# Performance work log

Measured on AMD Instinct MI355X. Metric: run time of the kernel, lower is better.

Reference implementation:

```python
import jax, jax.numpy as jnp
import numpy as np

B, L, D, N = 2, 2048, 1024, 16
HD = D // N  # head_dim = 64
EPS = 1e-5


def layer_norm(x, gamma, beta):
    mu = jnp.mean(x, axis=-1, keepdims=True)
    var = jnp.mean(jnp.square(x - mu), axis=-1, keepdims=True)
    return (x - mu) * jax.lax.rsqrt(var + EPS) * gamma + beta


def setup_inputs() -> dict:
    key = jax.random.key(0)
    ks = jax.random.split(key, 10)
    s = lambda fan_in: 1.0 / np.sqrt(fan_in)
    return {
        "x": jax.random.normal(ks[0], (B, L, D), dtype=jnp.float32),
        "wq": jax.random.uniform(ks[1], (D, D), jnp.float32, -s(D), s(D)),
        "wk": jax.random.uniform(ks[2], (D, D), jnp.float32, -s(D), s(D)),  # shared w_proj (k and v)
        "wo": jax.random.uniform(ks[3], (D, D), jnp.float32, -s(D), s(D)),
        "g1": jnp.ones((D,), jnp.float32),
        "b1": jnp.zeros((D,), jnp.float32),
        "w1": jax.random.uniform(ks[4], (D, 4 * D), jnp.float32, -s(D), s(D)),
        "bb1": jax.random.uniform(ks[5], (4 * D,), jnp.float32, -s(D), s(D)),
        "w2": jax.random.uniform(ks[6], (4 * D, D), jnp.float32, -s(4 * D), s(4 * D)),
        "bb2": jax.random.uniform(ks[7], (D,), jnp.float32, -s(4 * D), s(4 * D)),
        "g2": jnp.ones((D,), jnp.float32),
        "b2": jnp.zeros((D,), jnp.float32),
    }


def reference(x, wq, wk, wo, g1, b1, w1, bb1, w2, bb2, g2, b2):
    b, l, d = x.shape
    # projections (w_proj is shared for k and v in the source; v output is unused)
    q = (x @ wq).reshape(b, l, HD, N)
    k = (x @ wk).reshape(b, l, HD, N)
    # attention scores [b, l, m, n]; softmax over m (dim=2 in source)
    scores = jnp.einsum('bldn,bmdn->blmn', q, k) / np.sqrt(HD).astype(np.float32)
    attn = jax.nn.softmax(scores, axis=2)
    # NOTE: source contracts attention weights with K, not V (faithful bug reproduction)
    ctx = jnp.einsum('blmn,bmdn->bldn', attn, k).reshape(b, l, d)
    attn_out = ctx @ wo
    # post-LN residual block
    h = layer_norm(x + attn_out, g1, b1)
    ff = jax.nn.gelu(h @ w1 + bb1, approximate=False) @ w2 + bb2
    return layer_norm(h + ff, g2, b2)
```

## Files before the change

### kernel.cpp

```cpp
#include <hip/hip_runtime.h>
#include <math.h>

typedef unsigned short u16;
typedef unsigned int u32;
typedef __bf16 bf16x8 __attribute__((ext_vector_type(8)));
typedef unsigned short us8 __attribute__((ext_vector_type(8)));
typedef unsigned short us4 __attribute__((ext_vector_type(4)));
typedef float f32x4 __attribute__((ext_vector_type(4)));

#define DEV __device__ __forceinline__

DEV float fast_exp2(float x) { return __builtin_amdgcn_exp2f(x); }

DEV u16 f2bf(float f) {
  __bf16 h = (__bf16)f;
  return __builtin_bit_cast(u16, h);
}
DEV float bf2f(u16 h) { return __builtin_bit_cast(float, (u32)h << 16); }

DEV bf16x8 ld_bf8(const u16* p) { return __builtin_bit_cast(bf16x8, *(const us8*)p); }

DEV void gload_lds16(const u16* g, u16* l) {
  __builtin_amdgcn_global_load_lds((const __attribute__((address_space(1))) void*)g,
                                   (__attribute__((address_space(3))) void*)l, 16, 0, 0);
}

DEV f32x4 mfma16(bf16x8 a, bf16x8 b, f32x4 c) {
  return __builtin_amdgcn_mfma_f32_16x16x32_bf16(a, b, c, 0, 0, 0);
}

#define BAR __builtin_amdgcn_s_barrier()
#define LGK asm volatile("s_waitcnt lgkmcnt(0)" ::: "memory")
#define VM4 asm volatile("s_waitcnt vmcnt(4)" ::: "memory")


__global__ void conv_bf16_kernel(const float* __restrict__ in, u16* __restrict__ out, int n4) {
  const int stride = gridDim.x * blockDim.x;
  for (int i = blockIdx.x * blockDim.x + threadIdx.x; i < n4; i += stride) {
    float4 v = ((const float4*)in)[i];
    us4 h; h[0] = f2bf(v.x); h[1] = f2bf(v.y); h[2] = f2bf(v.z); h[3] = f2bf(v.w);
    ((us4*)out)[i] = h;
  }
}

template <int P>
__global__ __launch_bounds__(256) void transpose_bf16_kernel(
    const float* __restrict__ in, u16* __restrict__ out, int K, int N, float scale) {
  __shared__ float tile[32][33];
  const int nbk = K >> 5;
  const int bk = blockIdx.x % nbk, bn = blockIdx.x / nbk;
  const int r0 = bk << 5, c0 = bn << 5;
  const int t = threadIdx.x;
  {
    const int r = t >> 3, c4 = (t & 7) << 2;
    int sr = r0 + r;
    if constexpr (P == 2) sr = ((sr & 63) << 4) | (sr >> 6);
    const float4 v = *(const float4*)(in + (size_t)sr * N + c0 + c4);
    tile[r][c4] = v.x; tile[r][c4 + 1] = v.y; tile[r][c4 + 2] = v.z; tile[r][c4 + 3] = v.w;
  }
  __syncthreads();
  {
    const int oc = t >> 3, r4 = (t & 7) << 2;
    int orow = c0 + oc;
    if constexpr (P == 1) orow = ((orow & 15) << 6) | (orow >> 4);
    us4 h;
#pragma unroll
    for (int j = 0; j < 4; j++) h[j] = f2bf(tile[r4 + j][oc] * scale);
    *(us4*)(out + (size_t)orow * K + r0 + r4) = h;
  }
}

__global__ __launch_bounds__(256) void khead_transpose(
    const u16* __restrict__ qk, u16* __restrict__ kth) {
  __shared__ u16 tT[64 * 64];
  char* base = (char*)tT;
  const int t = threadIdx.x;
  const int bid = blockIdx.x;
  const int lt = bid & 31, n = (bid >> 5) & 15, b = bid >> 9;
#pragma unroll
  for (int rr = 0; rr < 2; rr++) {
    const int l = rr * 32 + (t >> 3);
    const int d0 = (t & 7) * 8;
    us8 v = *(const us8*)(qk + ((size_t)(b * 2048 + lt * 64 + l)) * 2048 + 1024 + n * 64 + d0);
#pragma unroll
    for (int j = 0; j < 8; j++) {
      const int d = d0 + j;
      *(u16*)(base + d * 128 + ((2 * l) ^ (16 * (d >> 3)))) = v[j];
    }
  }
  __syncthreads();
  const int w = t >> 6, lane = t & 63;
#pragma unroll
  for (int rr = 0; rr < 2; rr++) {
    const int d = rr * 32 + w * 8 + (lane >> 3);
    const int l = (lane & 7) * 8;
    us8 v = *(const us8*)(base + d * 128 + ((2 * l) ^ (16 * (d >> 3))));
    *(us8*)(kth + ((size_t)((b * 16 + n) * 64 + d)) * 2048 + lt * 64 + l) = v;
  }
}

template <int MODE, int BN>
__global__ __launch_bounds__(256) void gemm128(
    const u16* __restrict__ A, const u16* __restrict__ BT,
    int M, int N, int K,
    u16* __restrict__ ob, float* __restrict__ of, const float* __restrict__ res) {
  constexpr int NJ = BN / 32;
  constexpr int WCC = BN / 2;
  __shared__ u16 As[2][4096];
  __shared__ u16 Bs[2][BN * 32];
  const int t = threadIdx.x;
  const int nbm = M >> 7;
  const int nblk = nbm * (N / BN);
  int bid = blockIdx.x;
  bid = (bid & 7) * (nblk >> 3) + (bid >> 3);
  const int bm = bid % nbm;
  const int bn = bid / nbm;
  const int m0 = bm << 7, n0 = bn * BN;
  const int w = t >> 6, lane = t & 63;
  const int wr = w >> 1, wc = w & 1;
  const int lr = lane & 15, lg = lane >> 4, lq = (lane >> 4) << 2;
  const int rsw = (lg ^ (lr & 3)) << 3;

  const int srow = t >> 2;
  const int sseg = (t & 3) ^ (srow & 3);
  const u16* ap = A + (size_t)(m0 + srow) * K + sseg * 8;
  const u16* bp = BT + (size_t)(n0 + srow) * K + sseg * 8;
  const size_t half = (size_t)64 * K;

#define STAGE(buf, k0)                                                 \
  {                                                                    \
    gload_lds16(ap + (k0), &As[buf][t << 3]);                          \
    gload_lds16(ap + half + (k0), &As[buf][(t << 3) + 2048]);          \
    gload_lds16(bp + (k0), &Bs[buf][t << 3]);                          \
    if constexpr (BN == 128)                                           \
      gload_lds16(bp + half + (k0), &Bs[buf][(t << 3) + 2048]);        \
  }

  f32x4 acc[4][NJ];
#pragma unroll
  for (int i = 0; i < 4; i++)
#pragma unroll
    for (int j = 0; j < NJ; j++) acc[i][j] = (f32x4){0.f, 0.f, 0.f, 0.f};

  STAGE(0, 0);
  __syncthreads();
  const int NI = K >> 5;
  for (int it = 0; it < NI; ++it) {
    const int buf = it & 1;
    if (it + 1 < NI) STAGE(buf ^ 1, (it + 1) << 5);
    bf16x8 af[4], bfr[NJ];
#pragma unroll
    for (int i = 0; i < 4; i++)
      af[i] = ld_bf8(&As[buf][(wr * 64 + i * 16 + lr) * 32 + rsw]);
#pragma unroll
    for (int j = 0; j < NJ; j++)
      bfr[j] = ld_bf8(&Bs[buf][(wc * WCC + j * 16 + lr) * 32 + rsw]);
#pragma unroll
    for (int i = 0; i < 4; i++)
#pragma unroll
      for (int j = 0; j < NJ; j++) acc[i][j] = mfma16(af[i], bfr[j], acc[i][j]);
    __syncthreads();
  }
#undef STAGE

#pragma unroll
  for (int i = 0; i < 4; i++) {
    const int r0 = m0 + wr * 64 + i * 16 + lq;
#pragma unroll
    for (int j = 0; j < NJ; j++) {
      const int c = n0 + wc * WCC + j * 16 + lr;
      if constexpr (MODE == 0) {
#pragma unroll
        for (int q = 0; q < 4; q++) ob[(size_t)(r0 + q) * N + c] = f2bf(acc[i][j][q]);
      } else {
#pragma unroll
        for (int q = 0; q < 4; q++) {
          const size_t idx = (size_t)(r0 + q) * N + c;
          of[idx] = acc[i][j][q] + res[idx];
        }
      }
    }
  }
}

template <int MODE, int KS>
__global__ __launch_bounds__(512, 2) void gemm256(
    const u16* __restrict__ A, const u16* __restrict__ BT,
    int M, int N, int K,
    u16* __restrict__ ob, float* __restrict__ of, const float* __restrict__ bias) {
  __shared__ u16 AL[2][2][8192];
  __shared__ u16 BL[2][2][8192];
  const int t = threadIdx.x;
  const int lane = t & 63, wid = t >> 6;
  const int lr = lane & 15, lg = lane >> 4;
  const int wm = wid >> 2, wn = wid & 3;
  const int nbm = M >> 8, nbn = N >> 8;
  const int nblk = nbm * nbn * KS;
  int bid = blockIdx.x;
  bid = (bid & 7) * (nblk >> 3) + (bid >> 3);
  int ks = 0;
  if constexpr (KS > 1) { ks = bid % KS; bid /= KS; }
  const int bm = bid % nbm, bn = bid / nbm;
  const int m0 = bm << 8, n0 = bn << 8;
  const int KB = K / KS;
  const int NT = KB >> 6;
  const u16* Ag = A + (size_t)m0 * K + ks * KB;
  const u16* Bg = BT + (size_t)n0 * K + ks * KB;
  const int sseg = (t & 7) ^ (((t >> 5) & 1) << 1);
  const int akey = ((lr >> 2) & 1) << 1;

  auto stgA = [&](int buf, int h, int kt) {
    const u16* s = Ag + (size_t)(h * 128 + (t >> 3)) * K + kt * 64 + sseg * 8;
    gload_lds16(s, &AL[buf][h][t * 8]);
    gload_lds16(s + (size_t)64 * K, &AL[buf][h][4096 + t * 8]);
  };
  auto stgB = [&](int buf, int h, int kt) {
    const u16* s = Bg + (size_t)(h * 128 + (t >> 3)) * K + kt * 64 + sseg * 8;
    gload_lds16(s, &BL[buf][h][t * 8]);
    gload_lds16(s + (size_t)64 * K, &BL[buf][h][4096 + t * 8]);
  };

#define RDA(DST, BUF, IB)                                                      \
  _Pragma("unroll") for (int i4 = 0; i4 < 4; i4++)                             \
  _Pragma("unroll") for (int kk = 0; kk < 2; kk++)                             \
    DST[i4][kk] = ld_bf8(&AL[BUF][wm][((IB + i4) * 16 + lr) * 64 +             \
                                      ((kk * 4 + lg) ^ akey) * 8]);
#define RDB(DST, BUF, JB)                                                      \
  _Pragma("unroll") for (int j2 = 0; j2 < 2; j2++)                             \
  _Pragma("unroll") for (int kk = 0; kk < 2; kk++)                             \
    DST[j2][kk] = ld_bf8(&BL[BUF][wn >> 1][((wn & 1) * 64 + (JB + j2) * 16 +   \
                                            lr) * 64 +                         \
                                           ((kk * 4 + lg) ^ akey) * 8]);
#define QUAD(AF, BF, IB, JB)                                                   \
  __builtin_amdgcn_s_setprio(1);                                               \
  _Pragma("unroll") for (int i4 = 0; i4 < 4; i4++)                             \
  _Pragma("unroll") for (int j2 = 0; j2 < 2; j2++)                             \
  _Pragma("unroll") for (int kk = 0; kk < 2; kk++)                             \
    acc[IB + i4][JB + j2] = mfma16(AF[i4][kk], BF[j2][kk], acc[IB + i4][JB + j2]); \
  __builtin_amdgcn_s_setprio(0);

  f32x4 acc[8][4];
#pragma unroll
  for (int i = 0; i < 8; i++)
#pragma unroll
    for (int j = 0; j < 4; j++) acc[i][j] = (f32x4){0.f, 0.f, 0.f, 0.f};
  bf16x8 a0[4][2], a1[4][2], b0[2][2], b1[2][2];

  stgA(0, 0, 0); stgA(0, 1, 0); stgB(0, 0, 0); stgB(0, 1, 0);
  stgA(1, 0, 1); stgA(1, 1, 1);
  VM4;
  BAR;

  const int NI = NT >> 1;
  for (int it = 0; it < NI; ++it) {
    const int kt1 = 2 * it + 1;
    const int ktA = (2 * it + 2 < NT) ? 2 * it + 2 : NT - 1;
    const int ktB = (2 * it + 3 < NT) ? 2 * it + 3 : NT - 1;
    RDA(a0, 0, 0); RDB(b0, 0, 0); stgB(1, 0, kt1);
    BAR; QUAD(a0, b0, 0, 0); LGK; BAR;
    RDA(a1, 0, 4); stgB(1, 1, kt1);
    BAR; QUAD(a1, b0, 4, 0); LGK; BAR;
    RDB(b1, 0, 2); stgA(0, 0, ktA);
    BAR; QUAD(a1, b1, 4, 2); LGK; BAR;
    stgA(0, 1, ktA);
    BAR; QUAD(a0, b1, 0, 2); LGK; VM4; BAR;
    RDA(a0, 1, 0); RDB(b0, 1, 0); stgB(0, 0, ktA);
    BAR; QUAD(a0, b0, 0, 0); LGK; BAR;
    RDA(a1, 1, 4); stgB(0, 1, ktA);
    BAR; QUAD(a1, b0, 4, 0); LGK; BAR;
    RDB(b1, 1, 2); stgA(1, 0, ktB);
    BAR; QUAD(a1, b1, 4, 2); LGK; BAR;
    stgA(1, 1, ktB);
    BAR; QUAD(a0, b1, 0, 2); LGK; VM4; BAR;
  }
#undef RDA
#undef RDB
#undef QUAD

#pragma unroll
  for (int i = 0; i < 8; i++) {
    const int r = m0 + wm * 128 + i * 16 + lg * 4;
#pragma unroll
    for (int j = 0; j < 4; j++) {
      const int c = n0 + wn * 64 + j * 16 + lr;
      if constexpr (MODE == 0) {
        const float bv = bias[c];
#pragma unroll
        for (int q = 0; q < 4; q++) {
          float u = acc[i][j][q] + bv;
          ob[(size_t)(r + q) * N + c] = f2bf(0.5f * u * (1.f + erff(u * 0.70710678118f)));
        }
      } else {
        float* op = of + (size_t)ks * M * N;
#pragma unroll
        for (int q = 0; q < 4; q++) op[(size_t)(r + q) * N + c] = acc[i][j][q];
      }
    }
  }
}

__global__ __launch_bounds__(256, 2) void attn_kernel(
    const u16* __restrict__ qk, const u16* __restrict__ kth, u16* __restrict__ ctxh) {
  __shared__ u16 KsB[2][4096];
  __shared__ u16 KtsB[2][4096];
  __shared__ u16 Plds[4][2048];
  const int t = threadIdx.x, w = t >> 6, lane = t & 63;
  const int lr = lane & 15, lg = lane >> 4;
  int bid = blockIdx.x;
  bid = (bid & 7) * 64 + (bid >> 3);
  const int qb = bid & 15, hn = (bid >> 4) & 15, b = bid >> 8;
  const int lw = qb * 128 + w * 32;
  const u16* ksrc = qk + (size_t)b * 2048 * 2048 + 1024 + hn * 64;
  const u16* ktb = kth + ((size_t)(b * 16 + hn)) * 64 * 2048;
  char* pb = (char*)&Plds[w][0];
  const int swz = (lr & 7) << 4;

#define STAGE_KV(buf, m0s)                                                    \
  {                                                                           \
    _Pragma("unroll") for (int i_ = 0; i_ < 2; i_++) {                        \
      const int s_ = t + 256 * i_;                                            \
      const int row_ = s_ >> 3;                                               \
      const int c_ = (s_ & 7) ^ (row_ & 7);                                   \
      gload_lds16(ksrc + (size_t)((m0s) + row_) * 2048 + c_ * 8,              \
                  &KsB[buf][s_ * 8]);                                         \
      gload_lds16(ktb + (size_t)row_ * 2048 + (m0s) + c_ * 8,                 \
                  &KtsB[buf][s_ * 8]);                                        \
    }                                                                         \
  }

  bf16x8 qf[2][2];
#pragma unroll
  for (int f = 0; f < 2; f++)
#pragma unroll
    for (int kk = 0; kk < 2; kk++)
      qf[f][kk] = ld_bf8(qk + (size_t)(b * 2048 + lw + 16 * f + lr) * 2048 + hn * 64 +
                         kk * 32 + lg * 8);

  float mrow[2] = {-1e30f, -1e30f}, lrow[2] = {0.f, 0.f};
  f32x4 o[2][4];
#pragma unroll
  for (int f = 0; f < 2; f++)
#pragma unroll
    for (int dj = 0; dj < 4; dj++) o[f][dj] = (f32x4){0.f, 0.f, 0.f, 0.f};

  STAGE_KV(0, 0);
  __syncthreads();

  for (int it = 0; it < 32; ++it) {
    const int buf = it & 1;
    if (it < 31) STAGE_KV(buf ^ 1, (it + 1) * 64);

    f32x4 sc[2][4];
#pragma unroll
    for (int f = 0; f < 2; f++)
#pragma unroll
      for (int mj = 0; mj < 4; mj++) sc[f][mj] = (f32x4){0.f, 0.f, 0.f, 0.f};
#pragma unroll
    for (int mj = 0; mj < 4; mj++) {
      const int krow = 16 * mj + lr;
      bf16x8 kf0 = ld_bf8(&KsB[buf][krow * 64 + ((lg ^ (krow & 7)) << 3)]);
      bf16x8 kf1 = ld_bf8(&KsB[buf][krow * 64 + (((4 + lg) ^ (krow & 7)) << 3)]);
#pragma unroll
      for (int f = 0; f < 2; f++) {
        sc[f][mj] = mfma16(kf0, qf[f][0], sc[f][mj]);
        sc[f][mj] = mfma16(kf1, qf[f][1], sc[f][mj]);
      }
    }

#pragma unroll
    for (int f = 0; f < 2; f++) {
      float tm = fmaxf(fmaxf(sc[f][0][0], sc[f][0][1]), fmaxf(sc[f][0][2], sc[f][0][3]));
#pragma unroll
      for (int mj = 1; mj < 4; mj++)
        tm = fmaxf(tm, fmaxf(fmaxf(sc[f][mj][0], sc[f][mj][1]),
                             fmaxf(sc[f][mj][2], sc[f][mj][3])));
      tm = fmaxf(tm, __shfl_xor(tm, 16));
      tm = fmaxf(tm, __shfl_xor(tm, 32));
      if (!__all(tm <= mrow[f] + 8.f)) {
        const float mnew = fmaxf(mrow[f], tm);
        const float al = fast_exp2(mrow[f] - mnew);
        mrow[f] = mnew;
        lrow[f] *= al;
        float albc[4];
#pragma unroll
        for (int q = 0; q < 4; q++) albc[q] = __shfl(al, 4 * lg + q);
#pragma unroll
        for (int dj = 0; dj < 4; dj++)
#pragma unroll
          for (int q = 0; q < 4; q++) o[f][dj][q] *= albc[q];
      }
      float ts = 0.f;
      char* pf = pb + f * 2048;
#pragma unroll
      for (int mj = 0; mj < 4; mj++) {
        float p0 = fast_exp2(sc[f][mj][0] - mrow[f]);
        float p1 = fast_exp2(sc[f][mj][1] - mrow[f]);
        float p2 = fast_exp2(sc[f][mj][2] - mrow[f]);
        float p3 = fast_exp2(sc[f][mj][3] - mrow[f]);
        ts += (p0 + p1) + (p2 + p3);
        u32 w0 = (u32)f2bf(p0) | ((u32)f2bf(p1) << 16);
        u32 w1 = (u32)f2bf(p2) | ((u32)f2bf(p3) << 16);
        *(uint2*)(pf + ((lr * 128 + mj * 32 + lg * 8) ^ swz)) = make_uint2(w0, w1);
      }
      ts += __shfl_xor(ts, 16);
      ts += __shfl_xor(ts, 32);
      lrow[f] += ts;
    }

    bf16x8 pa[2][2];
#pragma unroll
    for (int f = 0; f < 2; f++)
#pragma unroll
      for (int kk = 0; kk < 2; kk++)
        pa[f][kk] = __builtin_bit_cast(
            bf16x8, *(const us8*)(pb + f * 2048 + ((lr * 128 + kk * 64 + lg * 16) ^ swz)));

#pragma unroll
    for (int dj = 0; dj < 4; dj++) {
      const int vrow = dj * 16 + lr;
      bf16x8 v0 = ld_bf8(&KtsB[buf][vrow * 64 + ((lg ^ (vrow & 7)) << 3)]);
      bf16x8 v1 = ld_bf8(&KtsB[buf][vrow * 64 + (((4 + lg) ^ (vrow & 7)) << 3)]);
#pragma unroll
      for (int f = 0; f < 2; f++) {
        o[f][dj] = mfma16(pa[f][0], v0, o[f][dj]);
        o[f][dj] = mfma16(pa[f][1], v1, o[f][dj]);
      }
    }
    __syncthreads();
  }
#undef STAGE_KV

#pragma unroll
  for (int f = 0; f < 2; f++) {
    const float inv = 1.f / lrow[f];
    float invbc[4];
#pragma unroll
    for (int q = 0; q < 4; q++) invbc[q] = __shfl(inv, 4 * lg + q);
#pragma unroll
    for (int q = 0; q < 4; q++) {
      const int ll = lw + 16 * f + 4 * lg + q;
#pragma unroll
      for (int dj = 0; dj < 4; dj++) {
        ctxh[((size_t)(b * 2048 + ll)) * 1024 + hn * 64 + dj * 16 + lr] =
            f2bf(o[f][dj][q] * invbc[q]);
      }
    }
  }
}

__global__ __launch_bounds__(256) void ln1_kernel(
    const float* __restrict__ in, const float* __restrict__ gamma,
    const float* __restrict__ beta, u16* __restrict__ o16) {
  __shared__ float red[8];
  const int row = blockIdx.x, t = threadIdx.x;
  const float4 v = ((const float4*)(in + (size_t)row * 1024))[t];
  float s = v.x + v.y + v.z + v.w;
  float ss = v.x * v.x + v.y * v.y + v.z * v.z + v.w * v.w;
#pragma unroll
  for (int off = 1; off < 64; off <<= 1) { s += __shfl_xor(s, off); ss += __shfl_xor(ss, off); }
  if ((t & 63) == 0) { red[t >> 6] = s; red[4 + (t >> 6)] = ss; }
  __syncthreads();
  const float st = red[0] + red[1] + red[2] + red[3];
  const float sst = red[4] + red[5] + red[6] + red[7];
  const float mean = st * (1.f / 1024.f);
  const float var = sst * (1.f / 1024.f) - mean * mean;
  const float rs = rsqrtf(var + 1e-5f);
  const float4 gv = ((const float4*)gamma)[t];
  const float4 bv = ((const float4*)beta)[t];
  us4 h;
  h[0] = f2bf((v.x - mean) * rs * gv.x + bv.x);
  h[1] = f2bf((v.y - mean) * rs * gv.y + bv.y);
  h[2] = f2bf((v.z - mean) * rs * gv.z + bv.z);
  h[3] = f2bf((v.w - mean) * rs * gv.w + bv.w);
  *(us4*)(o16 + (size_t)row * 1024 + t * 4) = h;
}

template <int NP>
__global__ __launch_bounds__(256) void ln2_kernel(
    const float* __restrict__ p, size_t pstride,
    const u16* __restrict__ resb, const float* __restrict__ bias,
    const float* __restrict__ gamma, const float* __restrict__ beta,
    float* __restrict__ o32) {
  __shared__ float red[8];
  const int row = blockIdx.x, t = threadIdx.x;
  float4 v = ((const float4*)(p + (size_t)row * 1024))[t];
#pragma unroll
  for (int k = 1; k < NP; k++) {
    const float4 v2 = ((const float4*)(p + (size_t)k * pstride + (size_t)row * 1024))[t];
    v.x += v2.x; v.y += v2.y; v.z += v2.z; v.w += v2.w;
  }
  {
    const us4 rb = *(const us4*)(resb + (size_t)row * 1024 + t * 4);
    const float4 vb = ((const float4*)bias)[t];
    v.x += bf2f(rb[0]) + vb.x;
    v.y += bf2f(rb[1]) + vb.y;
    v.z += bf2f(rb[2]) + vb.z;
    v.w += bf2f(rb[3]) + vb.w;
  }
  float s = v.x + v.y + v.z + v.w;
  float ss = v.x * v.x + v.y * v.y + v.z * v.z + v.w * v.w;
#pragma unroll
  for (int off = 1; off < 64; off <<= 1) { s += __shfl_xor(s, off); ss += __shfl_xor(ss, off); }
  if ((t & 63) == 0) { red[t >> 6] = s; red[4 + (t >> 6)] = ss; }
  __syncthreads();
  const float st = red[0] + red[1] + red[2] + red[3];
  const float sst = red[4] + red[5] + red[6] + red[7];
  const float mean = st * (1.f / 1024.f);
  const float var = sst * (1.f / 1024.f) - mean * mean;
  const float rs = rsqrtf(var + 1e-5f);
  const float4 gv = ((const float4*)gamma)[t];
  const float4 bv = ((const float4*)beta)[t];
  float4 ov;
  ov.x = (v.x - mean) * rs * gv.x + bv.x;
  ov.y = (v.y - mean) * rs * gv.y + bv.y;
  ov.z = (v.z - mean) * rs * gv.z + bv.z;
  ov.w = (v.w - mean) * rs * gv.w + bv.w;
  ((float4*)(o32 + (size_t)row * 1024))[t] = ov;
}

extern "C" void kernel_launch(void* const* d_in, const int* in_sizes, int n_in,
                              void* d_out, int out_size, void* d_ws, size_t ws_size,
                              hipStream_t stream) {
  const float* x   = (const float*)d_in[0];
  const float* wq  = (const float*)d_in[1];
  const float* wk  = (const float*)d_in[2];
  const float* wo  = (const float*)d_in[3];
  const float* g1  = (const float*)d_in[4];
  const float* b1  = (const float*)d_in[5];
  const float* w1  = (const float*)d_in[6];
  const float* bb1 = (const float*)d_in[7];
  const float* w2  = (const float*)d_in[8];
  const float* bb2 = (const float*)d_in[9];
  const float* g2  = (const float*)d_in[10];
  const float* b2  = (const float*)d_in[11];

  char* ws = (char*)d_ws;
  const size_t MB = 1ull << 20;
  u16* w2T   = (u16*)(ws + 0 * MB);
  u16* hb    = (u16*)(ws + 8 * MB);
  u16* tbuf  = (u16*)(ws + 16 * MB);
  float* rA  = (float*)(ws + 48 * MB);
  u16* wqkT  = (u16*)(ws + 26 * MB);
  u16* xb    = (u16*)(ws + 30 * MB);
  u16* qk    = (u16*)(ws + 38 * MB);
  u16* kthp  = (u16*)(ws + 54 * MB);
  u16* ctxh  = (u16*)(ws + 62 * MB);
  float* rbuf = (float*)(ws + 70 * MB);
  u16* w1T   = (u16*)(ws + 86 * MB);
  u16* woT   = (u16*)(ws + 94 * MB);

  const bool ks4 = ws_size >= 112 * MB;

  conv_bf16_kernel<<<1024, 256, 0, stream>>>(x, xb, 1048576);
  transpose_bf16_kernel<1><<<1024, 256, 0, stream>>>(wq, wqkT, 1024, 1024, 0.125f * 1.44269504089f);
  transpose_bf16_kernel<1><<<1024, 256, 0, stream>>>(wk, wqkT + (size_t)1024 * 1024, 1024, 1024, 1.0f);
  transpose_bf16_kernel<2><<<1024, 256, 0, stream>>>(wo, woT, 1024, 1024, 1.0f);
  transpose_bf16_kernel<0><<<32 * 128, 256, 0, stream>>>(w1, w1T, 1024, 4096, 1.0f);
  transpose_bf16_kernel<0><<<128 * 32, 256, 0, stream>>>(w2, w2T, 4096, 1024, 1.0f);

  gemm128<0, 128><<<32 * 16, 256, 0, stream>>>(xb, wqkT, 4096, 2048, 1024, qk, nullptr, nullptr);
  khead_transpose<<<1024, 256, 0, stream>>>(qk, kthp);

  attn_kernel<<<512, 256, 0, stream>>>(qk, kthp, ctxh);

  gemm128<2, 64><<<32 * 16, 256, 0, stream>>>(ctxh, woT, 4096, 1024, 1024, nullptr, rbuf, x);
  ln1_kernel<<<4096, 256, 0, stream>>>(rbuf, g1, b1, hb);

  gemm256<0, 1><<<256, 512, 0, stream>>>(hb, w1T, 4096, 4096, 1024, tbuf, nullptr, bb1);
  const size_t MN = (size_t)4096 * 1024;
  if (ks4) {
    gemm256<1, 4><<<256, 512, 0, stream>>>(tbuf, w2T, 4096, 1024, 4096, nullptr, rA, nullptr);
    ln2_kernel<4><<<4096, 256, 0, stream>>>(rA, MN, hb, bb2, g2, b2, (float*)d_out);
  } else {
    gemm256<1, 2><<<128, 512, 0, stream>>>(tbuf, w2T, 4096, 1024, 4096, nullptr, rA, nullptr);
    ln2_kernel<2><<<4096, 256, 0, stream>>>(rA, MN, hb, bb2, g2, b2, (float*)d_out);
  }
}
```

Measured before the change: 267.1 us.

## Split attention KV range across two blocks with combine pass; use gemm256 for QK

The attention kernel now splits each query block's key range into two halves handled by separate blocks. Each block writes unnormalized partial outputs plus per-row max and sum statistics, and a new combine kernel merges the two halves with log-sum-exp weights. This doubles the grid to fill the GPU better, and the P scratch buffer is shrunk so occupancy can be raised to 4 blocks per SM. The QK projection also moves to the gemm256 kernel through a new bf16-output mode. The cost is an extra kernel launch plus a round trip of partial outputs through memory, with one bf16 rounding of the partial outputs before the merge.

Measured after the change: 274.9 us. 2.9% more time.

```diff
diff --git a/kernel.cpp b/kernel.cpp
--- a/kernel.cpp
+++ b/kernel.cpp
@@ -290,26 +290,31 @@
           float u = acc[i][j][q] + bv;
           ob[(size_t)(r + q) * N + c] = f2bf(0.5f * u * (1.f + erff(u * 0.70710678118f)));
         }
+      } else if constexpr (MODE == 1) {
+        float* op = of + (size_t)ks * M * N;
+#pragma unroll
+        for (int q = 0; q < 4; q++) op[(size_t)(r + q) * N + c] = acc[i][j][q];
       } else {
-        float* op = of + (size_t)ks * M * N;
-#pragma unroll
-        for (int q = 0; q < 4; q++) op[(size_t)(r + q) * N + c] = acc[i][j][q];
+#pragma unroll
+        for (int q = 0; q < 4; q++) ob[(size_t)(r + q) * N + c] = f2bf(acc[i][j][q]);
       }
     }
   }
 }
 
-__global__ __launch_bounds__(256, 2) void attn_kernel(
-    const u16* __restrict__ qk, const u16* __restrict__ kth, u16* __restrict__ ctxh) {
+__global__ __launch_bounds__(256, 4) void attn_kernel(
+    const u16* __restrict__ qk, const u16* __restrict__ kth,
+    u16* __restrict__ op, float* __restrict__ stat) {
   __shared__ u16 KsB[2][4096];
   __shared__ u16 KtsB[2][4096];
-  __shared__ u16 Plds[4][2048];
+  __shared__ u16 Plds[4][1024];
   const int t = threadIdx.x, w = t >> 6, lane = t & 63;
   const int lr = lane & 15, lg = lane >> 4;
   int bid = blockIdx.x;
-  bid = (bid & 7) * 64 + (bid >> 3);
-  const int qb = bid & 15, hn = (bid >> 4) & 15, b = bid >> 8;
+  bid = (bid & 7) * 128 + (bid >> 3);
+  const int kv = bid & 1, qb = (bid >> 1) & 15, hn = (bid >> 5) & 15, b = bid >> 9;
   const int lw = qb * 128 + w * 32;
+  const int m00 = kv * 1024;
   const u16* ksrc = qk + (size_t)b * 2048 * 2048 + 1024 + hn * 64;
   const u16* ktb = kth + ((size_t)(b * 16 + hn)) * 64 * 2048;
   char* pb = (char*)&Plds[w][0];
@@ -343,12 +348,12 @@
 #pragma unroll
     for (int dj = 0; dj < 4; dj++) o[f][dj] = (f32x4){0.f, 0.f, 0.f, 0.f};
 
-  STAGE_KV(0, 0);
+  STAGE_KV(0, m00);
   __syncthreads();
 
-  for (int it = 0; it < 32; ++it) {
+  for (int it = 0; it < 16; ++it) {
     const int buf = it & 1;
-    if (it < 31) STAGE_KV(buf ^ 1, (it + 1) * 64);
+    if (it < 15) STAGE_KV(buf ^ 1, m00 + (it + 1) * 64);
 
     f32x4 sc[2][4];
 #pragma unroll
@@ -367,6 +372,7 @@
       }
     }
 
+    bf16x8 pa[2][2];
 #pragma unroll
     for (int f = 0; f < 2; f++) {
       float tm = fmaxf(fmaxf(sc[f][0][0], sc[f][0][1]), fmaxf(sc[f][0][2], sc[f][0][3]));
@@ -390,7 +396,6 @@
           for (int q = 0; q < 4; q++) o[f][dj][q] *= albc[q];
       }
       float ts = 0.f;
-      char* pf = pb + f * 2048;
 #pragma unroll
       for (int mj = 0; mj < 4; mj++) {
         float p0 = fast_exp2(sc[f][mj][0] - mrow[f]);
@@ -400,20 +405,16 @@
         ts += (p0 + p1) + (p2 + p3);
         u32 w0 = (u32)f2bf(p0) | ((u32)f2bf(p1) << 16);
         u32 w1 = (u32)f2bf(p2) | ((u32)f2bf(p3) << 16);
-        *(uint2*)(pf + ((lr * 128 + mj * 32 + lg * 8) ^ swz)) = make_uint2(w0, w1);
+        *(uint2*)(pb + ((lr * 128 + mj * 32 + lg * 8) ^ swz)) = make_uint2(w0, w1);
       }
       ts += __shfl_xor(ts, 16);
       ts += __shfl_xor(ts, 32);
       lrow[f] += ts;
-    }
-
-    bf16x8 pa[2][2];
-#pragma unroll
-    for (int f = 0; f < 2; f++)
 #pragma unroll
       for (int kk = 0; kk < 2; kk++)
         pa[f][kk] = __builtin_bit_cast(
-            bf16x8, *(const us8*)(pb + f * 2048 + ((lr * 128 + kk * 64 + lg * 16) ^ swz)));
+            bf16x8, *(const us8*)(pb + ((lr * 128 + kk * 64 + lg * 16) ^ swz)));
+    }
 
 #pragma unroll
     for (int dj = 0; dj < 4; dj++) {
@@ -430,22 +431,43 @@
   }
 #undef STAGE_KV
 
+  u16* ob = op + (size_t)kv * 4096 * 1024;
 #pragma unroll
   for (int f = 0; f < 2; f++) {
-    const float inv = 1.f / lrow[f];
-    float invbc[4];
-#pragma unroll
-    for (int q = 0; q < 4; q++) invbc[q] = __shfl(inv, 4 * lg + q);
 #pragma unroll
     for (int q = 0; q < 4; q++) {
       const int ll = lw + 16 * f + 4 * lg + q;
 #pragma unroll
       for (int dj = 0; dj < 4; dj++) {
-        ctxh[((size_t)(b * 2048 + ll)) * 1024 + hn * 64 + dj * 16 + lr] =
-            f2bf(o[f][dj][q] * invbc[q]);
+        ob[((size_t)(b * 2048 + ll)) * 1024 + hn * 64 + dj * 16 + lr] = f2bf(o[f][dj][q]);
       }
     }
-  }
+    if (lg == 0) {
+      const int sidx = (b * 16 + hn) * 2048 + lw + 16 * f + lr;
+      stat[kv * 131072 + sidx] = mrow[f];
+      stat[kv * 131072 + 65536 + sidx] = lrow[f];
+    }
+  }
+}
+
+__global__ __launch_bounds__(256) void attn_combine(
+    const u16* __restrict__ op, const float* __restrict__ stat, u16* __restrict__ ctxh) {
+  const int row = blockIdx.x, t = threadIdx.x;
+  const int hn = t >> 4;
+  const int b = row >> 11, l = row & 2047;
+  const int sidx = (b * 16 + hn) * 2048 + l;
+  const float m0 = stat[sidx], l0 = stat[65536 + sidx];
+  const float m1 = stat[131072 + sidx], l1 = stat[196608 + sidx];
+  const float mm = fmaxf(m0, m1);
+  const float w0 = fast_exp2(m0 - mm), w1 = fast_exp2(m1 - mm);
+  const float inv = 1.f / (w0 * l0 + w1 * l1);
+  const float s0 = w0 * inv, s1 = w1 * inv;
+  const us4 a = *(const us4*)(op + (size_t)row * 1024 + t * 4);
+  const us4 c = *(const us4*)(op + (size_t)(4096 + row) * 1024 + t * 4);
+  us4 h;
+#pragma unroll
+  for (int j = 0; j < 4; j++) h[j] = f2bf(bf2f(a[j]) * s0 + bf2f(c[j]) * s1);
+  *(us4*)(ctxh + (size_t)row * 1024 + t * 4) = h;
 }
 
 __global__ __launch_bounds__(256) void ln1_kernel(
@@ -538,16 +560,18 @@
   const size_t MB = 1ull << 20;
   u16* w2T   = (u16*)(ws + 0 * MB);
   u16* hb    = (u16*)(ws + 8 * MB);
+  u16* obuf  = (u16*)(ws + 16 * MB);
+  float* stat = (float*)(ws + 32 * MB);
   u16* tbuf  = (u16*)(ws + 16 * MB);
   float* rA  = (float*)(ws + 48 * MB);
   u16* wqkT  = (u16*)(ws + 26 * MB);
-  u16* xb    = (u16*)(ws + 30 * MB);
-  u16* qk    = (u16*)(ws + 38 * MB);
-  u16* kthp  = (u16*)(ws + 54 * MB);
-  u16* ctxh  = (u16*)(ws + 62 * MB);
-  float* rbuf = (float*)(ws + 70 * MB);
-  u16* w1T   = (u16*)(ws + 86 * MB);
-  u16* woT   = (u16*)(ws + 94 * MB);
+  u16* xb    = (u16*)(ws + 33 * MB);
+  u16* qk    = (u16*)(ws + 41 * MB);
+  u16* kthp  = (u16*)(ws + 57 * MB);
+  u16* ctxh  = (u16*)(ws + 65 * MB);
+  float* rbuf = (float*)(ws + 73 * MB);
+  u16* w1T   = (u16*)(ws + 89 * MB);
+  u16* woT   = (u16*)(ws + 97 * MB);
 
   const bool ks4 = ws_size >= 112 * MB;
 
@@ -558,10 +582,11 @@
   transpose_bf16_kernel<0><<<32 * 128, 256, 0, stream>>>(w1, w1T, 1024, 4096, 1.0f);
   transpose_bf16_kernel<0><<<128 * 32, 256, 0, stream>>>(w2, w2T, 4096, 1024, 1.0f);
 
-  gemm128<0, 128><<<32 * 16, 256, 0, stream>>>(xb, wqkT, 4096, 2048, 1024, qk, nullptr, nullptr);
+  gemm256<2, 1><<<128, 512, 0, stream>>>(xb, wqkT, 4096, 2048, 1024, qk, nullptr, nullptr);
   khead_transpose<<<1024, 256, 0, stream>>>(qk, kthp);
 
-  attn_kernel<<<512, 256, 0, stream>>>(qk, kthp, ctxh);
+  attn_kernel<<<1024, 256, 0, stream>>>(qk, kthp, obuf, stat);
+  attn_combine<<<4096, 256, 0, stream>>>(obuf, stat, ctxh);
 
   gemm128<2, 64><<<32 * 16, 256, 0, stream>>>(ctxh, woT, 4096, 1024, 1024, nullptr, rbuf, x);
   ln1_kernel<<<4096, 256, 0, stream>>>(rbuf, g1, b1, hb);
```
